# Optimization experiments

Hardware: AMD Instinct MI355X
Metric: run time of the kernel (lower is better)

The kernel has to match this reference:

```python
import jax, jax.numpy as jnp
import numpy as np

NODE_SIZE = 100000
DIM = 512
B = 2048
GAMMA = 3.0
LAMB = 20.0
TAU = 8.0


def setup_inputs() -> dict:
    key = jax.random.key(0)
    k1, k2 = jax.random.split(key)
    pairs = jax.random.randint(k1, (B, 2), 0, NODE_SIZE, dtype=jnp.int64 if jax.config.jax_enable_x64 else jnp.int32)
    emb = jax.random.normal(k2, (NODE_SIZE, DIM), dtype=jnp.float32)
    return {"pairs": pairs, "emb": emb}


def _align_loss(pairs, emb):
    l = pairs[:, 0]
    r = pairs[:, 1]
    l_emb = emb[l]                     # [B, D]
    r_emb = emb[r]                     # [B, D]
    pos_dis = jnp.sum(jnp.square(l_emb - r_emb), axis=-1, keepdims=True)  # [B, 1]

    emb_sq = jnp.sum(jnp.square(emb), axis=1)          # [N]

    def squared_dist(A):
        # ||a||^2 + ||b||^2 - 2 a.b  -> [B, N]
        a_sq = jnp.sum(jnp.square(A), axis=1, keepdims=True)
        return a_sq + emb_sq[None, :] - 2.0 * (A @ emb.T)

    l_neg_dis = squared_dist(l_emb)
    r_neg_dis = squared_dist(r_emb)

    # mask = 1 - one_hot(l) - one_hot(r), built without materializing one-hots
    rows = jnp.arange(B)
    mask = jnp.ones((B, NODE_SIZE), dtype=emb.dtype)
    mask = mask.at[rows, l].add(-1.0)
    mask = mask.at[rows, r].add(-1.0)

    def norm_lse(loss):
        loss = loss * mask
        mu = jax.lax.stop_gradient(jnp.mean(loss, axis=-1, keepdims=True))
        sd = jax.lax.stop_gradient(jnp.std(loss, axis=-1, keepdims=True))  # unbiased=False
        loss = (loss - mu) / sd
        return jax.scipy.special.logsumexp(LAMB * loss + TAU, axis=-1)

    l_loss = norm_lse(pos_dis - l_neg_dis + GAMMA)
    r_loss = norm_lse(pos_dis - r_neg_dis + GAMMA)
    return jnp.mean(l_loss + r_loss)


def reference(pairs, emb):
    return _align_loss(pairs, emb)
```

## Files before the change

kernel.cpp:

```cpp
#include <hip/hip_runtime.h>
#include <stdint.h>

#define NODES   100000
#define NPAD    100096
#define DIM     512
#define NPAIR   2048
#define MROWS   4096
#define NBLK    391
#define MTILES  16
#define GAMMA_F 3.0f
#define LAMB_F  20.0f
#define TAU_F   8.0f
#define SHIFT_F 140.0f

#define BM 256
#define BN 256
#define BK 64

typedef __attribute__((ext_vector_type(8))) short          short8;
typedef __attribute__((ext_vector_type(8))) unsigned short ushort8;
typedef __attribute__((ext_vector_type(4))) float          f32x4;


__device__ __forceinline__ unsigned short f2bf(float f) {
    unsigned u = __float_as_uint(f);
    u += 0x7FFFu + ((u >> 16) & 1u);
    return (unsigned short)(u >> 16);
}
__device__ __forceinline__ float bf2f(unsigned short h) {
    return __uint_as_float(((unsigned)h) << 16);
}

__device__ __forceinline__ void gload_lds16(const void* g, void* l) {
    unsigned lofs = (unsigned)__builtin_amdgcn_readfirstlane((unsigned)(uintptr_t)l);
    auto lp = reinterpret_cast<__attribute__((address_space(3))) unsigned*>(lofs);
    auto gp = (const __attribute__((address_space(1))) unsigned*)g;
    __builtin_amdgcn_global_load_lds(gp, lp, 16, 0, 0);
}


__global__ void convert_stats_kernel(const float* __restrict__ emb,
                                     unsigned short* __restrict__ Ebf,
                                     float* __restrict__ esq,
                                     float* __restrict__ Spart,
                                     float* __restrict__ Tpart,
                                     float* __restrict__ E1part,
                                     float* __restrict__ E2part) {
    __shared__ float Sl[4][512];
    __shared__ float Tl[4][512];
    __shared__ float ew[8];
    const int b = blockIdx.x, t = threadIdx.x;
    const int lane = t & 63, wave = t >> 6;
    const int r0 = b * 196;
    float sacc[8], tacc[8];
    #pragma unroll
    for (int k = 0; k < 8; ++k) { sacc[k] = 0.f; tacc[k] = 0.f; }
    float e1 = 0.f, e2 = 0.f;
    for (int i = 0; i < 49; ++i) {
        const int row = r0 + i * 4 + wave;
        if (row >= NPAD) continue;
        const bool real = row < NODES;
        float v[8];
        float ss = 0.f;
        if (real) {
            const float4* p = (const float4*)(emb + (size_t)row * DIM + lane * 8);
            float4 a = p[0], bb = p[1];
            v[0]=a.x; v[1]=a.y; v[2]=a.z; v[3]=a.w;
            v[4]=bb.x; v[5]=bb.y; v[6]=bb.z; v[7]=bb.w;
            #pragma unroll
            for (int k = 0; k < 8; ++k) ss += v[k] * v[k];
        } else {
            #pragma unroll
            for (int k = 0; k < 8; ++k) v[k] = 0.f;
        }
        #pragma unroll
        for (int o = 1; o < 64; o <<= 1) ss += __shfl_xor(ss, o);
        ushort8 o8;
        float vr[8];
        #pragma unroll
        for (int k = 0; k < 8; ++k) { o8[k] = f2bf(v[k]); vr[k] = bf2f(o8[k]); }
        *(ushort8*)(Ebf + (size_t)row * DIM + lane * 8) = o8;
        if (lane == 0) esq[row] = ss;
        if (real) {
            #pragma unroll
            for (int k = 0; k < 8; ++k) { sacc[k] += vr[k]; tacc[k] += ss * vr[k]; }
            if (lane == 0) { e1 += ss; e2 += ss * ss; }
        }
    }
    #pragma unroll
    for (int k = 0; k < 8; ++k) {
        Sl[wave][lane * 8 + k] = sacc[k];
        Tl[wave][lane * 8 + k] = tacc[k];
    }
    if (lane == 0) { ew[wave] = e1; ew[4 + wave] = e2; }
    __syncthreads();
    #pragma unroll
    for (int kk = 0; kk < 2; ++kk) {
        const int d = 2 * t + kk;
        Spart[(size_t)b * 512 + d] = Sl[0][d] + Sl[1][d] + Sl[2][d] + Sl[3][d];
        Tpart[(size_t)b * 512 + d] = Tl[0][d] + Tl[1][d] + Tl[2][d] + Tl[3][d];
    }
    if (t == 0) E1part[b] = ew[0] + ew[1] + ew[2] + ew[3];
    if (t == 1) E2part[b] = ew[4] + ew[5] + ew[6] + ew[7];
}

__global__ void stats_merge_kernel(const float* __restrict__ Spart,
                                   const float* __restrict__ Tpart,
                                   const float* __restrict__ E1part,
                                   const float* __restrict__ E2part,
                                   float* __restrict__ Svec,
                                   float* __restrict__ Tvec,
                                   double* __restrict__ E12) {
    const int t = threadIdx.x;
    if (t < 512) {
        float s = 0.f;
        for (int b = 0; b < 512; ++b) s += Spart[(size_t)b * 512 + t];
        Svec[t] = s;
    } else {
        const int d = t - 512;
        float s = 0.f;
        for (int b = 0; b < 512; ++b) s += Tpart[(size_t)b * 512 + d];
        Tvec[d] = s;
    }
    if (t == 0) { double a = 0.0; for (int b = 0; b < 512; ++b) a += (double)E1part[b]; E12[0] = a; }
    if (t == 1) { double a = 0.0; for (int b = 0; b < 512; ++b) a += (double)E2part[b]; E12[1] = a; }
}

__global__ void gather_kernel(const int* __restrict__ pairs,
                              const float* __restrict__ emb,
                              unsigned short* __restrict__ Abf,
                              float* __restrict__ cvec,
                              float* __restrict__ posv) {
    const int p    = blockIdx.x;
    const int lane = threadIdx.x;
    const int li = pairs[2 * p], ri = pairs[2 * p + 1];
    const float4* pl = (const float4*)(emb + (size_t)li * DIM + lane * 8);
    const float4* pr = (const float4*)(emb + (size_t)ri * DIM + lane * 8);
    float4 a0 = pl[0], a1 = pl[1];
    float4 b0 = pr[0], b1 = pr[1];
    float la[8] = {a0.x,a0.y,a0.z,a0.w,a1.x,a1.y,a1.z,a1.w};
    float lb[8] = {b0.x,b0.y,b0.z,b0.w,b1.x,b1.y,b1.z,b1.w};
    float sa = 0.f, sb = 0.f, sd = 0.f;
    ushort8 oa, ob;
    #pragma unroll
    for (int i = 0; i < 8; ++i) {
        sa += la[i] * la[i];
        sb += lb[i] * lb[i];
        float d = la[i] - lb[i];
        sd += d * d;
        oa[i] = f2bf(la[i]);
        ob[i] = f2bf(lb[i]);
    }
    *(ushort8*)(Abf + (size_t)p * DIM + lane * 8)            = oa;
    *(ushort8*)(Abf + (size_t)(NPAIR + p) * DIM + lane * 8)  = ob;
    #pragma unroll
    for (int off = 1; off < 64; off <<= 1) {
        sa += __shfl_xor(sa, off);
        sb += __shfl_xor(sb, off);
        sd += __shfl_xor(sd, off);
    }
    if (lane == 0) {
        cvec[p]         = sd - sa + GAMMA_F;
        cvec[NPAIR + p] = sd - sb + GAMMA_F;
        posv[p]         = sd;
    }
}


__launch_bounds__(256, 2)
__global__ void gram_kernel(const unsigned short* __restrict__ Ebf,
                            float* __restrict__ Gpart) {
    __shared__ unsigned short ldsA[64 * 128];
    __shared__ unsigned short ldsB[64 * 128];
    const int tid  = threadIdx.x;
    const int lane = tid & 63;
    const int wave = tid >> 6;
    const int wx = wave & 1, wy = wave >> 1;
    const int d1base = blockIdx.y * 128;
    const int d2base = blockIdx.x * 128;
    const int bz = blockIdx.z;
    const int r15 = lane & 15, q = lane >> 4;

    f32x4 zero4 = {0.f, 0.f, 0.f, 0.f};
    f32x4 acc[4][4];
    #pragma unroll
    for (int i = 0; i < 4; ++i)
        #pragma unroll
        for (int j = 0; j < 4; ++j) acc[i][j] = zero4;

    for (int jc = bz; jc < NPAD / 64; jc += 32) {
        const int j0 = jc * 64;
        #pragma unroll
        for (int ii = 0; ii < 4; ++ii) {
            const int iss = wave * 4 + ii;
            const int row = iss * 4 + (lane >> 4);
            gload_lds16(Ebf + (size_t)(j0 + row) * DIM + d1base + (lane & 15) * 8,
                        &ldsA[iss * 4 * 128]);
            gload_lds16(Ebf + (size_t)(j0 + row) * DIM + d2base + (lane & 15) * 8,
                        &ldsB[iss * 4 * 128]);
        }
        __builtin_amdgcn_s_waitcnt(0);
        __syncthreads();
        #pragma unroll
        for (int h = 0; h < 2; ++h) {
            short8 af[4], bfv[4];
            #pragma unroll
            for (int mt = 0; mt < 4; ++mt) {
                const int m = wy * 64 + mt * 16 + r15;
                #pragma unroll
                for (int i = 0; i < 8; ++i)
                    af[mt][i] = (short)ldsA[(h * 32 + q * 8 + i) * 128 + m];
            }
            #pragma unroll
            for (int nt = 0; nt < 4; ++nt) {
                const int n = wx * 64 + nt * 16 + r15;
                #pragma unroll
                for (int i = 0; i < 8; ++i)
                    bfv[nt][i] = (short)ldsB[(h * 32 + q * 8 + i) * 128 + n];
            }
            #pragma unroll
            for (int mt = 0; mt < 4; ++mt)
                #pragma unroll
                for (int nt = 0; nt < 4; ++nt)
                    acc[mt][nt] = __builtin_amdgcn_mfma_f32_16x16x32_bf16(
                        af[mt], bfv[nt], acc[mt][nt], 0, 0, 0);
        }
        __syncthreads();
    }
    float* gp = Gpart + (size_t)bz * 512 * 512;
    #pragma unroll
    for (int mt = 0; mt < 4; ++mt)
        #pragma unroll
        for (int r = 0; r < 4; ++r) {
            const int d1 = d1base + wy * 64 + mt * 16 + q * 4 + r;
            #pragma unroll
            for (int nt = 0; nt < 4; ++nt) {
                const int d2 = d2base + wx * 64 + nt * 16 + r15;
                gp[d1 * 512 + d2] = acc[mt][nt][r];
            }
        }
}

__global__ void gram_merge_kernel(const float* __restrict__ Gpart,
                                  float* __restrict__ G) {
    const int idx = blockIdx.x * 256 + threadIdx.x;
    float s = 0.f;
    for (int b = 0; b < 32; ++b) s += Gpart[(size_t)b * 512 * 512 + idx];
    G[idx] = s;
}


__launch_bounds__(256)
__global__ void gu_kernel(const unsigned short* __restrict__ Abf,
                          const float* __restrict__ G,
                          const float* __restrict__ Svec,
                          const float* __restrict__ Tvec,
                          const double* __restrict__ E12,
                          const float* __restrict__ cvec,
                          const float* __restrict__ posv,
                          const int* __restrict__ pairs,
                          float* __restrict__ alpha_v,
                          float* __restrict__ shift_v) {
    __shared__ float u[8][512];
    __shared__ float red[8][3][4];
    const int t = threadIdx.x;
    const int lane = t & 63, wave = t >> 6;
    const int r0 = blockIdx.x * 8;
    #pragma unroll
    for (int p = 0; p < 8; ++p) {
        unsigned pk = *(const unsigned*)(Abf + (size_t)(r0 + p) * DIM + 2 * t);
        u[p][2 * t]     = bf2f((unsigned short)(pk & 0xffffu));
        u[p][2 * t + 1] = bf2f((unsigned short)(pk >> 16));
    }
    __syncthreads();
    float acc0[8], acc1[8];
    #pragma unroll
    for (int p = 0; p < 8; ++p) { acc0[p] = 0.f; acc1[p] = 0.f; }
    for (int d1 = 0; d1 < 512; ++d1) {
        const float2 g = *(const float2*)(G + d1 * 512 + 2 * t);
        #pragma unroll
        for (int p = 0; p < 8; ++p) {
            const float up = u[p][d1];
            acc0[p] += up * g.x;
            acc1[p] += up * g.y;
        }
    }
    const float sv0 = Svec[2 * t], sv1 = Svec[2 * t + 1];
    const float tv0 = Tvec[2 * t], tv1 = Tvec[2 * t + 1];
    #pragma unroll
    for (int p = 0; p < 8; ++p) {
        const float u0 = u[p][2 * t], u1 = u[p][2 * t + 1];
        float pdS = u0 * sv0 + u1 * sv1;
        float pdT = u0 * tv0 + u1 * tv1;
        float pq  = u0 * acc0[p] + u1 * acc1[p];
        #pragma unroll
        for (int off = 1; off < 64; off <<= 1) {
            pdS += __shfl_xor(pdS, off);
            pdT += __shfl_xor(pdT, off);
            pq  += __shfl_xor(pq,  off);
        }
        if (lane == 0) {
            red[p][0][wave] = pdS;
            red[p][1][wave] = pdT;
            red[p][2][wave] = pq;
        }
    }
    __syncthreads();
    if (t < 8) {
        const int p = t;
        const double dS = (double)red[p][0][0] + red[p][0][1] + red[p][0][2] + red[p][0][3];
        const double dT = (double)red[p][1][0] + red[p][1][1] + red[p][1][2] + red[p][1][3];
        const double qq = (double)red[p][2][0] + red[p][2][1] + red[p][2][2] + red[p][2][3];
        const int row = r0 + p;
        const int pp  = row & (NPAIR - 1);
        const double c  = (double)cvec[row];
        const double E1 = E12[0], E2 = E12[1];
        const double N  = (double)NODES;
        double Sx  = N * c + 2.0 * dS - E1;
        double Sxx = (N * c * c - 2.0 * c * E1 + E2) + 4.0 * (c * dS - dT) + 4.0 * qq;
        const int li = pairs[2 * pp], ri = pairs[2 * pp + 1];
        const double pos = (double)posv[pp];
        if (li != ri) {
            const double x1 = pos + (double)GAMMA_F, x2 = (double)GAMMA_F;
            Sx  -= x1 + x2;
            Sxx -= x1 * x1 + x2 * x2;
        } else {
            Sx -= 2.0 * (double)GAMMA_F;
        }
        const double mu  = Sx / N;
        const double var = Sxx / N - mu * mu;
        const double sd  = sqrt(fmax(var, 1e-30));
        const double al  = (double)LAMB_F / sd;
        alpha_v[row] = (float)al;
        shift_v[row] = (float)(al * mu + (double)SHIFT_F);
    }
}


__device__ __forceinline__ void stage_band(const unsigned short* __restrict__ tile,
                                           int band, unsigned short* ldsbuf,
                                           int kb, int lane, int wave) {
    const int r  = wave * 8 + (lane >> 3);
    const int ch = (lane & 7) ^ (r & 7);
    gload_lds16(tile + (size_t)(band * 64 + r) * DIM + kb + ch * 8,
                ldsbuf + ((size_t)band * 64 + wave * 8) * BK);
}

template<int H, int MH>
__device__ __forceinline__ void read_a(const unsigned short* lA, int wr, int r15,
                                       int q, short8 afr[4]) {
    #pragma unroll
    for (int mt4 = 0; mt4 < 4; ++mt4) {
        const int row = wr * 128 + MH * 64 + mt4 * 16 + r15;
        const int c   = (H * 4 + q) ^ (row & 7);
        afr[mt4] = *(const short8*)&lA[row * BK + c * 8];
    }
}
template<int H>
__device__ __forceinline__ void read_b(const unsigned short* lB, int wc, int r15,
                                       int q, short8 bfr[4]) {
    #pragma unroll
    for (int nt = 0; nt < 4; ++nt) {
        const int row = wc * 64 + nt * 16 + r15;
        const int c   = (H * 4 + q) ^ (row & 7);
        bfr[nt] = *(const short8*)&lB[row * BK + c * 8];
    }
}
template<int MH>
__device__ __forceinline__ void do_mfma(const short8 afr[4], const short8 bfr[4],
                                        f32x4 (&acc)[8][4]) {
    __builtin_amdgcn_s_setprio(1);
    #pragma unroll
    for (int mt4 = 0; mt4 < 4; ++mt4)
        #pragma unroll
        for (int nt = 0; nt < 4; ++nt)
            acc[MH * 4 + mt4][nt] = __builtin_amdgcn_mfma_f32_16x16x32_bf16(
                afr[mt4], bfr[nt], acc[MH * 4 + mt4][nt], 0, 0, 0);
    __builtin_amdgcn_s_setprio(0);
}

#define VMCNT2() asm volatile("s_waitcnt vmcnt(2)" ::: "memory")
#define VMCNT0() asm volatile("s_waitcnt vmcnt(0)" ::: "memory")
#define SBAR()   __builtin_amdgcn_s_barrier()

__launch_bounds__(512, 2)
__global__ void gemm_kernel(const unsigned short* __restrict__ Abf,
                            const unsigned short* __restrict__ Ebf,
                            const float* __restrict__ cvec,
                            const float* __restrict__ esq,
                            const int*   __restrict__ pairs,
                            const float* __restrict__ alpha_v,
                            const float* __restrict__ shift_v,
                            float* __restrict__ psum) {
    __shared__ unsigned short ldsA[2][BM * BK];
    __shared__ unsigned short ldsB[2][BN * BK];
    __shared__ float red_s[4][BM];
    __shared__ float alsh[BM], csh[BM], cmsh[BM];
    __shared__ int   lish[BM], rish[BM];

    const int tid  = threadIdx.x;
    const int lane = tid & 63;
    const int wave = tid >> 6;
    const int wr   = wave >> 2;
    const int wc   = wave & 3;
    const int r15  = lane & 15;
    const int q    = lane >> 4;

    const int bid = blockIdx.y * NBLK + blockIdx.x;
    const int swz = (bid & 7) * 782 + (bid >> 3);
    const int nb  = swz % NBLK;
    const int mp  = swz / NBLK;
    const int n0  = nb * BN;
    const int m0  = mp * BM;

    if (tid < BM) {
        const int gm = m0 + tid;
        alsh[tid] = alpha_v[gm];
        csh[tid]  = shift_v[gm];
        cmsh[tid] = cvec[gm];
        const int p = gm & (NPAIR - 1);
        lish[tid] = pairs[2 * p];
        rish[tid] = pairs[2 * p + 1];
    }
    __syncthreads();

    const unsigned short* Arow = Abf + (size_t)m0 * DIM;
    const unsigned short* Brow = Ebf + (size_t)n0 * DIM;

    f32x4 acc[8][4];
    #pragma unroll
    for (int i = 0; i < 8; ++i)
        #pragma unroll
        for (int j = 0; j < 4; ++j) acc[i][j] = (f32x4){0.f, 0.f, 0.f, 0.f};

    stage_band(Brow, 0, ldsB[0], 0, lane, wave);
    stage_band(Brow, 1, ldsB[0], 0, lane, wave);
    stage_band(Brow, 2, ldsB[0], 0, lane, wave);
    stage_band(Brow, 3, ldsB[0], 0, lane, wave);
    stage_band(Arow, 0, ldsA[0], 0, lane, wave);
    stage_band(Arow, 2, ldsA[0], 0, lane, wave);
    stage_band(Arow, 1, ldsA[0], 0, lane, wave);
    stage_band(Arow, 3, ldsA[0], 0, lane, wave);
    VMCNT2();
    SBAR();

    short8 afr[4], bfr[4];

    for (int kt = 0; kt < 7; ++kt) {
        unsigned short* lA  = ldsA[kt & 1];
        unsigned short* lB  = ldsB[kt & 1];
        unsigned short* lAn = ldsA[(kt & 1) ^ 1];
        unsigned short* lBn = ldsB[(kt & 1) ^ 1];
        const int kb2 = (kt + 1) * BK;

        read_a<0, 0>(lA, wr, r15, q, afr);
        read_b<0>(lB, wc, r15, q, bfr);
        stage_band(Brow, 0, lBn, kb2, lane, wave);
        stage_band(Brow, 1, lBn, kb2, lane, wave);
        SBAR();
        do_mfma<0>(afr, bfr, acc);
        VMCNT2();
        SBAR();
        read_a<0, 1>(lA, wr, r15, q, afr);
        stage_band(Brow, 2, lBn, kb2, lane, wave);
        stage_band(Brow, 3, lBn, kb2, lane, wave);
        SBAR();
        do_mfma<1>(afr, bfr, acc);
        SBAR();
        read_a<1, 0>(lA, wr, r15, q, afr);
        read_b<1>(lB, wc, r15, q, bfr);
        stage_band(Arow, 0, lAn, kb2, lane, wave);
        stage_band(Arow, 2, lAn, kb2, lane, wave);
        SBAR();
        do_mfma<0>(afr, bfr, acc);
        SBAR();
        read_a<1, 1>(lA, wr, r15, q, afr);
        stage_band(Arow, 1, lAn, kb2, lane, wave);
        stage_band(Arow, 3, lAn, kb2, lane, wave);
        SBAR();
        do_mfma<1>(afr, bfr, acc);
        VMCNT2();
        SBAR();
    }
    {
        unsigned short* lA = ldsA[1];
        unsigned short* lB = ldsB[1];
        read_a<0, 0>(lA, wr, r15, q, afr);
        read_b<0>(lB, wc, r15, q, bfr);
        SBAR();
        do_mfma<0>(afr, bfr, acc);
        VMCNT0();
        SBAR();
        read_a<0, 1>(lA, wr, r15, q, afr);
        SBAR();
        do_mfma<1>(afr, bfr, acc);
        SBAR();
        read_a<1, 0>(lA, wr, r15, q, afr);
        read_b<1>(lB, wc, r15, q, bfr);
        SBAR();
        do_mfma<0>(afr, bfr, acc);
        SBAR();
        read_a<1, 1>(lA, wr, r15, q, afr);
        SBAR();
        do_mfma<1>(afr, bfr, acc);
    }

    float eqv[4];
    int   gnv[4];
    #pragma unroll
    for (int nt = 0; nt < 4; ++nt) {
        const int gn = n0 + wc * 64 + nt * 16 + r15;
        gnv[nt] = gn;
        eqv[nt] = esq[gn];
    }
    #pragma unroll
    for (int mt = 0; mt < 8; ++mt) {
        #pragma unroll
        for (int r = 0; r < 4; ++r) {
            const int rit = wr * 128 + mt * 16 + q * 4 + r;
            const float cm = cmsh[rit];
            const float al = alsh[rit];
            const float Cc = csh[rit];
            const int li = lish[rit], ri = rish[rit];
            float se = 0.f;
            #pragma unroll
            for (int nt = 0; nt < 4; ++nt) {
                float xv = cm + 2.0f * acc[mt][nt][r] - eqv[nt];
                float msk = 1.0f - (float)(gnv[nt] == li) - (float)(gnv[nt] == ri);
                xv *= msk;
                float term = __expf(fmaf(al, xv, -Cc));
                se += (gnv[nt] < NODES) ? term : 0.f;
            }
            #pragma unroll
            for (int o = 1; o < 16; o <<= 1) se += __shfl_xor(se, o);
            if (r15 == 0) red_s[wc][rit] = se;
        }
    }
    __syncthreads();
    if (tid < BM) {
        psum[(size_t)nb * MROWS + m0 + tid] =
            red_s[0][tid] + red_s[1][tid] + red_s[2][tid] + red_s[3][tid];
    }
}


__global__ void lse_part_kernel(const float* __restrict__ psum,
                                float* __restrict__ lsep) {
    const int row = blockIdx.x * 256 + threadIdx.x;
    const int c   = blockIdx.y;
    const int nb0 = c * 98;
    const int nb1 = (nb0 + 98 < NBLK) ? nb0 + 98 : NBLK;
    float s = 0.f;
    for (int nb = nb0; nb < nb1; ++nb)
        s += psum[(size_t)nb * MROWS + row];
    lsep[(size_t)c * MROWS + row] = s;
}

__global__ void loss_kernel(const float* __restrict__ lsep,
                            float* __restrict__ loss_v) {
    const int row = blockIdx.x * 256 + threadIdx.x;
    const float s = lsep[row] + lsep[MROWS + row]
                  + lsep[2 * MROWS + row] + lsep[3 * MROWS + row];
    loss_v[row] = (TAU_F + SHIFT_F) + logf(s);
}

__global__ void final_kernel(const float* __restrict__ loss_v,
                             float* __restrict__ out) {
    __shared__ double wpart[4];
    int t = threadIdx.x;
    double s = 0.0;
    for (int i = t; i < MROWS; i += 256)
        s += (double)loss_v[i];
    #pragma unroll
    for (int off = 1; off < 64; off <<= 1) s += __shfl_xor(s, off);
    if ((t & 63) == 0) wpart[t >> 6] = s;
    __syncthreads();
    if (t == 0) out[0] = (float)((wpart[0] + wpart[1] + wpart[2] + wpart[3]) / (double)NPAIR);
}


extern "C" void kernel_launch(void* const* d_in, const int* in_sizes, int n_in,
                              void* d_out, int out_size, void* d_ws, size_t ws_size,
                              hipStream_t stream) {
    const int*   pairs = (const int*)d_in[0];
    const float* emb   = (const float*)d_in[1];
    float* out = (float*)d_out;

    char* ws = (char*)d_ws;
    size_t off = 0;
    auto alloc = [&](size_t bytes) -> void* {
        void* p = ws + off;
        off += (bytes + 255) & ~(size_t)255;
        return p;
    };
    unsigned short* Ebf = (unsigned short*)alloc((size_t)NPAD * DIM * 2);
    unsigned short* Abf = (unsigned short*)alloc((size_t)MROWS * DIM * 2);
    float*  esq     = (float*)alloc((size_t)NPAD * 4);
    float*  cvec    = (float*)alloc((size_t)MROWS * 4);
    float*  posv    = (float*)alloc((size_t)NPAIR * 4);
    float*  Spart   = (float*)alloc((size_t)512 * DIM * 4);
    float*  Tpart   = (float*)alloc((size_t)512 * DIM * 4);
    float*  E1part  = (float*)alloc((size_t)512 * 4);
    float*  E2part  = (float*)alloc((size_t)512 * 4);
    float*  Svec    = (float*)alloc((size_t)DIM * 4);
    float*  Tvec    = (float*)alloc((size_t)DIM * 4);
    double* E12     = (double*)alloc(2 * sizeof(double));
    float*  G       = (float*)alloc((size_t)512 * 512 * 4);
    float*  alpha_v = (float*)alloc((size_t)MROWS * 4);
    float*  shift_v = (float*)alloc((size_t)MROWS * 4);
    float*  lsep    = (float*)alloc((size_t)4 * MROWS * 4);
    float*  loss_v  = (float*)alloc((size_t)MROWS * 4);
    char* uni = (char*)alloc((size_t)32 * 512 * 512 * 4);
    float* Gpart = (float*)uni;
    float* psum  = (float*)uni;
    if (off > ws_size) return;

    convert_stats_kernel<<<512, 256, 0, stream>>>(emb, Ebf, esq,
                                                  Spart, Tpart, E1part, E2part);
    stats_merge_kernel<<<1, 1024, 0, stream>>>(Spart, Tpart, E1part, E2part,
                                               Svec, Tvec, E12);
    gather_kernel<<<NPAIR, 64, 0, stream>>>(pairs, emb, Abf, cvec, posv);

    gram_kernel<<<dim3(4, 4, 32), 256, 0, stream>>>(Ebf, Gpart);
    gram_merge_kernel<<<1024, 256, 0, stream>>>(Gpart, G);
    gu_kernel<<<MROWS / 8, 256, 0, stream>>>(Abf, G, Svec, Tvec, E12,
                                             cvec, posv, pairs, alpha_v, shift_v);

    gemm_kernel<<<dim3(NBLK, MTILES), 512, 0, stream>>>(Abf, Ebf, cvec, esq, pairs,
                                                        alpha_v, shift_v, psum);
    lse_part_kernel<<<dim3(16, 4), 256, 0, stream>>>(psum, lsep);
    loss_kernel<<<16, 256, 0, stream>>>(lsep, loss_v);
    final_kernel<<<1, 256, 0, stream>>>(loss_v, out);
}
```

Before: 1.126 ms.

## Issue all next-tile global loads up front and keep both B fragment halves in registers

Restructures the GEMM main loop so all eight global-to-LDS stage loads for the next K tile are issued at the start of each iteration instead of being spread across four phases. Both B fragment halves are now held in registers (bfr0/bfr1), so B is read from LDS once per tile, and the MFMA phases are reordered to sweep K halves first. Per-thread LDS offsets are precomputed once outside the loop. This raises memory-level parallelism and drops some address math and B reloads, at the cost of extra VGPRs under a 512-thread, 2-block launch bound, which could cause spills or lower occupancy.

New measurement: 1.165 ms. +3.5%, slower.

```diff
diff --git a/kernel.cpp b/kernel.cpp
--- a/kernel.cpp
+++ b/kernel.cpp
@@ -346,26 +346,13 @@
                 ldsbuf + ((size_t)band * 64 + wave * 8) * BK);
 }
 
-template<int H, int MH>
-__device__ __forceinline__ void read_a(const unsigned short* lA, int wr, int r15,
-                                       int q, short8 afr[4]) {
-    #pragma unroll
-    for (int mt4 = 0; mt4 < 4; ++mt4) {
-        const int row = wr * 128 + MH * 64 + mt4 * 16 + r15;
-        const int c   = (H * 4 + q) ^ (row & 7);
-        afr[mt4] = *(const short8*)&lA[row * BK + c * 8];
-    }
-}
-template<int H>
-__device__ __forceinline__ void read_b(const unsigned short* lB, int wc, int r15,
-                                       int q, short8 bfr[4]) {
-    #pragma unroll
-    for (int nt = 0; nt < 4; ++nt) {
-        const int row = wc * 64 + nt * 16 + r15;
-        const int c   = (H * 4 + q) ^ (row & 7);
-        bfr[nt] = *(const short8*)&lB[row * BK + c * 8];
-    }
-}
+__device__ __forceinline__ void read_frags4(const unsigned short* lds,
+                                            const int (&offs)[4], short8 out[4]) {
+    #pragma unroll
+    for (int i = 0; i < 4; ++i)
+        out[i] = *(const short8*)&lds[offs[i]];
+}
+
 template<int MH>
 __device__ __forceinline__ void do_mfma(const short8 afr[4], const short8 bfr[4],
                                         f32x4 (&acc)[8][4]) {
@@ -379,6 +366,7 @@
     __builtin_amdgcn_s_setprio(0);
 }
 
+#define VMCNT8() asm volatile("s_waitcnt vmcnt(8)" ::: "memory")
 #define VMCNT2() asm volatile("s_waitcnt vmcnt(2)" ::: "memory")
 #define VMCNT0() asm volatile("s_waitcnt vmcnt(0)" ::: "memory")
 #define SBAR()   __builtin_amdgcn_s_barrier()
@@ -427,6 +415,24 @@
     const unsigned short* Arow = Abf + (size_t)m0 * DIM;
     const unsigned short* Brow = Ebf + (size_t)n0 * DIM;
 
+    int aoff[2][2][4];
+    int boff[2][4];
+    #pragma unroll
+    for (int H = 0; H < 2; ++H) {
+        #pragma unroll
+        for (int MH = 0; MH < 2; ++MH)
+            #pragma unroll
+            for (int mt4 = 0; mt4 < 4; ++mt4) {
+                const int row = wr * 128 + MH * 64 + mt4 * 16 + r15;
+                aoff[H][MH][mt4] = row * BK + (((H * 4 + q) ^ (row & 7)) * 8);
+            }
+        #pragma unroll
+        for (int nt = 0; nt < 4; ++nt) {
+            const int row = wc * 64 + nt * 16 + r15;
+            boff[H][nt] = row * BK + (((H * 4 + q) ^ (row & 7)) * 8);
+        }
+    }
+
     f32x4 acc[8][4];
     #pragma unroll
     for (int i = 0; i < 8; ++i)
@@ -444,65 +450,65 @@
     VMCNT2();
     SBAR();
 
-    short8 afr[4], bfr[4];
+    short8 afr[4], bfr0[4], bfr1[4];
 
     for (int kt = 0; kt < 7; ++kt) {
-        unsigned short* lA  = ldsA[kt & 1];
-        unsigned short* lB  = ldsB[kt & 1];
+        const unsigned short* lA = ldsA[kt & 1];
+        const unsigned short* lB = ldsB[kt & 1];
         unsigned short* lAn = ldsA[(kt & 1) ^ 1];
         unsigned short* lBn = ldsB[(kt & 1) ^ 1];
         const int kb2 = (kt + 1) * BK;
 
-        read_a<0, 0>(lA, wr, r15, q, afr);
-        read_b<0>(lB, wc, r15, q, bfr);
+        read_frags4(lA, aoff[0][0], afr);
+        read_frags4(lB, boff[0],    bfr0);
         stage_band(Brow, 0, lBn, kb2, lane, wave);
         stage_band(Brow, 1, lBn, kb2, lane, wave);
-        SBAR();
-        do_mfma<0>(afr, bfr, acc);
-        VMCNT2();
-        SBAR();
-        read_a<0, 1>(lA, wr, r15, q, afr);
         stage_band(Brow, 2, lBn, kb2, lane, wave);
         stage_band(Brow, 3, lBn, kb2, lane, wave);
-        SBAR();
-        do_mfma<1>(afr, bfr, acc);
-        SBAR();
-        read_a<1, 0>(lA, wr, r15, q, afr);
-        read_b<1>(lB, wc, r15, q, bfr);
         stage_band(Arow, 0, lAn, kb2, lane, wave);
         stage_band(Arow, 2, lAn, kb2, lane, wave);
-        SBAR();
-        do_mfma<0>(afr, bfr, acc);
-        SBAR();
-        read_a<1, 1>(lA, wr, r15, q, afr);
         stage_band(Arow, 1, lAn, kb2, lane, wave);
         stage_band(Arow, 3, lAn, kb2, lane, wave);
         SBAR();
-        do_mfma<1>(afr, bfr, acc);
+        do_mfma<0>(afr, bfr0, acc);
+        SBAR();
+        read_frags4(lA, aoff[1][0], afr);
+        read_frags4(lB, boff[1],    bfr1);
+        SBAR();
+        do_mfma<0>(afr, bfr1, acc);
+        VMCNT8();
+        SBAR();
+        read_frags4(lA, aoff[0][1], afr);
+        SBAR();
+        do_mfma<1>(afr, bfr0, acc);
+        SBAR();
+        read_frags4(lA, aoff[1][1], afr);
+        SBAR();
+        do_mfma<1>(afr, bfr1, acc);
         VMCNT2();
         SBAR();
     }
     {
-        unsigned short* lA = ldsA[1];
-        unsigned short* lB = ldsB[1];
-        read_a<0, 0>(lA, wr, r15, q, afr);
-        read_b<0>(lB, wc, r15, q, bfr);
-        SBAR();
-        do_mfma<0>(afr, bfr, acc);
+        const unsigned short* lA = ldsA[1];
+        const unsigned short* lB = ldsB[1];
+        read_frags4(lA, aoff[0][0], afr);
+        read_frags4(lB, boff[0],    bfr0);
+        SBAR();
+        do_mfma<0>(afr, bfr0, acc);
+        SBAR();
+        read_frags4(lA, aoff[1][0], afr);
+        read_frags4(lB, boff[1],    bfr1);
+        SBAR();
+        do_mfma<0>(afr, bfr1, acc);
         VMCNT0();
         SBAR();
-        read_a<0, 1>(lA, wr, r15, q, afr);
-        SBAR();
-        do_mfma<1>(afr, bfr, acc);
-        SBAR();
-        read_a<1, 0>(lA, wr, r15, q, afr);
-        read_b<1>(lB, wc, r15, q, bfr);
-        SBAR();
-        do_mfma<0>(afr, bfr, acc);
-        SBAR();
-        read_a<1, 1>(lA, wr, r15, q, afr);
-        SBAR();
-        do_mfma<1>(afr, bfr, acc);
+        read_frags4(lA, aoff[0][1], afr);
+        SBAR();
+        do_mfma<1>(afr, bfr0, acc);
+        SBAR();
+        read_frags4(lA, aoff[1][1], afr);
+        SBAR();
+        do_mfma<1>(afr, bfr1, acc);
     }
 
     float eqv[4];
```
